# Kernel tuning notes

Hardware: AMD Instinct MI355X
Metric: run time of the kernel (lower is better)

Reference implementation:

```python
import jax, jax.numpy as jnp
import numpy as np

HID = 128
MAX_NODES = 100000
MAX_EDGES = 300000
EVT_LEN = 4096
NUM_NODE = 20000
NUM_EDGE = 320000
# EVENT_TYPE_ID_MAP: pad=0 start=1 end=2 node-add=3 node-delete=4 edge-add=5 edge-delete=6
NODE_ADD, NODE_DEL = 3, 4


def time_encode(t, time_w, time_b):
    # TimeEncoder: cos(Linear(1 -> hidden)(t))
    return jnp.cos(t[..., None] * time_w + time_b)


def gru_cell(x, h, w_ih, w_hh, b_ih, b_hh):
    gi = x @ w_ih.T + b_ih
    gh = h @ w_hh.T + b_hh
    i_r, i_z, i_n = jnp.split(gi, 3, axis=-1)
    h_r, h_z, h_n = jnp.split(gh, 3, axis=-1)
    r = jax.nn.sigmoid(i_r + h_r)
    z = jax.nn.sigmoid(i_z + h_z)
    n = jnp.tanh(i_n + r * h_n)
    return (1.0 - z) * n + z * h


def setup_inputs() -> dict:
    key = jax.random.key(0)
    ks = jax.random.split(key, 32)
    H = HID
    s = 0.05
    inp = {}
    inp["event_type_ids"] = jax.random.randint(ks[0], (EVT_LEN,), 0, 7)
    inp["src_ids"] = jax.random.randint(ks[1], (EVT_LEN,), 0, MAX_NODES)
    inp["src_mask"] = (jax.random.uniform(ks[2], (EVT_LEN,)) > 0.3).astype(jnp.float32)
    inp["dst_ids"] = jax.random.randint(ks[3], (EVT_LEN,), 0, MAX_NODES)
    inp["dst_mask"] = (jax.random.uniform(ks[4], (EVT_LEN,)) > 0.3).astype(jnp.float32)
    inp["event_edge_ids"] = jax.random.randint(ks[5], (EVT_LEN,), 0, MAX_EDGES)
    inp["event_embeddings"] = jax.random.normal(ks[6], (EVT_LEN, H), dtype=jnp.float32)
    inp["event_mask"] = (jax.random.uniform(ks[7], (EVT_LEN,)) > 0.2).astype(jnp.float32)
    inp["event_timestamps"] = jax.random.uniform(ks[8], (EVT_LEN,)) * 100.0
    inp["node_ids"] = jax.random.randint(ks[9], (NUM_NODE,), 0, MAX_NODES)
    inp["edge_ids"] = jax.random.randint(ks[10], (NUM_EDGE,), 0, MAX_EDGES)
    inp["edge_index"] = jax.random.randint(ks[11], (2, NUM_EDGE), 0, NUM_NODE)
    inp["time"] = 100
    # persistent-buffer state
    inp["memory"] = jax.random.normal(ks[12], (MAX_NODES, H), dtype=jnp.float32) * s
    inp["last_update"] = jax.random.uniform(ks[13], (MAX_EDGES,)) * 50.0
    inp["node_features"] = jax.random.normal(ks[14], (MAX_NODES, H), dtype=jnp.float32) * s
    inp["edge_features"] = jax.random.normal(ks[15], (MAX_EDGES, H), dtype=jnp.float32) * s
    # TimeEncoder params (Linear(1, H))
    inp["time_w"] = jax.random.normal(ks[16], (H,), dtype=jnp.float32) * s
    inp["time_b"] = jax.random.normal(ks[17], (H,), dtype=jnp.float32) * s
    # GRUCell(5H -> H)
    inp["gru_w_ih"] = jax.random.normal(ks[18], (3 * H, 5 * H), dtype=jnp.float32) * s
    inp["gru_w_hh"] = jax.random.normal(ks[19], (3 * H, H), dtype=jnp.float32) * s
    inp["gru_b_ih"] = jax.random.normal(ks[20], (3 * H,), dtype=jnp.float32) * s
    inp["gru_b_hh"] = jax.random.normal(ks[21], (3 * H,), dtype=jnp.float32) * s
    # TransformerConv(H, H, heads=1, edge_dim=2H)
    inp["wq"] = jax.random.normal(ks[22], (H, H), dtype=jnp.float32) * s
    inp["bq"] = jax.random.normal(ks[23], (H,), dtype=jnp.float32) * s
    inp["wk"] = jax.random.normal(ks[24], (H, H), dtype=jnp.float32) * s
    inp["bk"] = jax.random.normal(ks[25], (H,), dtype=jnp.float32) * s
    inp["wv"] = jax.random.normal(ks[26], (H, H), dtype=jnp.float32) * s
    inp["bv"] = jax.random.normal(ks[27], (H,), dtype=jnp.float32) * s
    inp["we"] = jax.random.normal(ks[28], (H, 2 * H), dtype=jnp.float32) * s  # lin_edge, no bias
    inp["wskip"] = jax.random.normal(ks[29], (H, H), dtype=jnp.float32) * s
    inp["bskip"] = jax.random.normal(ks[30], (H,), dtype=jnp.float32) * s
    return inp


def reference(event_type_ids, src_ids, src_mask, dst_ids, dst_mask, event_edge_ids,
              event_embeddings, event_mask, event_timestamps, node_ids, edge_ids,
              edge_index, time, memory, last_update, node_features, edge_features,
              time_w, time_b, gru_w_ih, gru_w_hh, gru_b_ih, gru_b_hh,
              wq, bq, wk, bk, wv, bv, we, wskip, bskip):
    H = HID
    # ---- message() ----
    L = event_type_ids.shape[0]
    type_embs = jnp.broadcast_to(event_type_ids[:, None].astype(memory.dtype), (L, H))
    src_embs = memory[src_ids] * src_mask[:, None]
    dst_embs = memory[dst_ids] * dst_mask[:, None]
    edge_last = last_update[event_edge_ids]
    rel_ts = event_timestamps - edge_last * dst_mask
    is_node_ev = ((event_type_ids == NODE_ADD) | (event_type_ids == NODE_DEL)).astype(event_timestamps.dtype)
    ts_emb = time_encode(event_timestamps * is_node_ev + rel_ts * dst_mask, time_w, time_b) * event_mask[:, None]
    src_msgs = jnp.concatenate([type_embs, src_embs, dst_embs, ts_emb, event_embeddings], axis=1) * event_mask[:, None]
    dst_msgs = jnp.concatenate([type_embs, dst_embs, src_embs, ts_emb, event_embeddings], axis=1) * dst_mask[:, None]
    # ---- agg_message(): scatter-mean over node ids ----
    def agg(msgs, ids):
        s = jax.ops.segment_sum(msgs, ids, num_segments=MAX_NODES)
        c = jax.ops.segment_sum(jnp.ones((msgs.shape[0],), msgs.dtype), ids, num_segments=MAX_NODES)
        return s / jnp.maximum(c, 1.0)[:, None]
    agg_src = agg(src_msgs, src_ids)
    agg_dst = agg(dst_msgs, dst_ids)
    # ---- GRU memory update on unique ids ----
    # torch: memory[cat(uniq_src, uniq_dst)] = rnn(...); reads use pre-update memory,
    # dst writes come after src writes so they override on overlap. Duplicate ids in
    # src_ids carry identical per-id values, so scatter-set is equivalent to unique().
    new_src = gru_cell(agg_src[src_ids], memory[src_ids], gru_w_ih, gru_w_hh, gru_b_ih, gru_b_hh)
    new_dst = gru_cell(agg_dst[dst_ids], memory[dst_ids], gru_w_ih, gru_w_hh, gru_b_ih, gru_b_hh)
    memory = memory.at[src_ids].set(new_src)
    memory = memory.at[dst_ids].set(new_dst)
    # ---- edge attributes ----
    rel_t = time - last_update[edge_ids]
    rel_t_embs = time_encode(rel_t, time_w, time_b)
    edge_attr = jnp.concatenate([rel_t_embs, edge_features[edge_ids]], axis=-1)  # (E, 2H)
    # ---- TransformerConv (heads=1, concat, root_weight) ----
    x = node_features[node_ids] + memory[node_ids]  # (N, H)
    src, dst = edge_index[0], edge_index[1]
    q = x @ wq.T + bq
    k = x @ wk.T + bk
    v = x @ wv.T + bv
    e = edge_attr @ we.T  # lin_edge (no bias)
    alpha = jnp.sum(q[dst] * (k[src] + e), axis=-1) / jnp.sqrt(jnp.asarray(H, x.dtype))
    amax = jax.ops.segment_max(alpha, dst, num_segments=x.shape[0])
    ex = jnp.exp(alpha - amax[dst])
    denom = jax.ops.segment_sum(ex, dst, num_segments=x.shape[0])
    p = ex / jnp.maximum(denom[dst], 1e-16)
    out = jax.ops.segment_sum(p[:, None] * (v[src] + e), dst, num_segments=x.shape[0])
    return out + x @ wskip.T + bskip
```

## Files before the change

kernel.cpp:

```cpp
#include <hip/hip_runtime.h>
#include <math.h>

#define HID   128
#define MAXN  100000
#define MAXE  300000
#define EVT   4096
#define NNODE 20000
#define NEDGE 320000

typedef unsigned short u16;
typedef __attribute__((ext_vector_type(8))) short bf16x8;
typedef __attribute__((ext_vector_type(4))) float f32x4;

#define OFF_WCATB     0u
#define OFF_WEB       589824u
#define OFF_WALLB     655360u
#define OFF_BALL      851968u
#define BASE2         855040u
#define OFF_HEAD_SRC  (BASE2 + 0u)
#define OFF_HEAD_DST  (BASE2 + 400128u)
#define OFF_CNT_SRC   (BASE2 + 800256u)
#define OFF_CNT_DST   (BASE2 + 1200384u)
#define OFF_CHAIN_SRC (BASE2 + 1600512u)
#define OFF_CHAIN_DST (BASE2 + 1616896u)
#define OFF_XHB       (BASE2 + 1703936u)
#define OFF_HG        (BASE2 + 14286848u)
#define OFF_XB        (BASE2 + 20000000u)
#define OFF_QB        (BASE2 + 25120000u)
#define OFF_SKIPF     (BASE2 + 55840000u)
#define OFF_DEG       (BASE2 + 66080000u)
#define OFF_OFFS      (BASE2 + 66160128u)
#define OFF_CURSOR    (BASE2 + 66240256u)
#define OFF_SORTED    (BASE2 + 66320384u)
#define OFF_SACCB     (BASE2 + 67600384u)

__device__ __forceinline__ float sigmoidf_(float x) { return 1.f / (1.f + __expf(-x)); }
__device__ __forceinline__ u16 f2b(float f) {
    unsigned u = __float_as_uint(f);
    unsigned r = (u + 0x7fffu + ((u >> 16) & 1u)) >> 16;
    return (u16)r;
}
__device__ __forceinline__ float b2f(unsigned h) { return __uint_as_float(h << 16); }

__global__ void k_prep(const float* __restrict__ w_ih, const float* __restrict__ w_hh,
                       const float* __restrict__ we,
                       const float* __restrict__ wq, const float* __restrict__ wk_,
                       const float* __restrict__ wv, const float* __restrict__ wskip,
                       const float* __restrict__ bq, const float* __restrict__ bk,
                       const float* __restrict__ bv, const float* __restrict__ bskip,
                       u16* __restrict__ Wcatb, u16* __restrict__ we_b,
                       u16* __restrict__ Wallb, float* __restrict__ ball,
                       int* __restrict__ deg, char* __restrict__ zbase) {
    int b = blockIdx.x, t = threadIdx.x;
    if (b < 1152) {
        int idx = b * 256 + t;
        int row = idx / 768, col = idx % 768;
        float v = (col < 640) ? w_ih[row * 640 + col] : w_hh[row * 128 + (col - 640)];
        Wcatb[idx] = f2b(v);
        return;
    }
    b -= 1152;
    if (b < 128) {
        int i = b * 256 + t;
        we_b[i] = f2b(we[i]);
        return;
    }
    b -= 128;
    if (b < 79) {
        int i = b * 256 + t;
        if (i < NNODE) deg[i] = 0;
        return;
    }
    b -= 79;
    if (b < 384) {
        int idx = b * 256 + t;
        int row = idx >> 7;
        int k = idx & 127;
        float v;
        if (row < 128)      v = wq[row * 128 + k];
        else if (row < 256) v = wk_[(row - 128) * 128 + k];
        else if (row < 384) v = wv[(row - 256) * 128 + k];
        else if (row < 512) v = wskip[(row - 384) * 128 + k];
        else {
            int j = row - 512;
            float a = 0.f;
            for (int t2 = 0; t2 < 128; t2++) a += wq[t2 * 128 + k] * we[t2 * 256 + j];
            v = a;
        }
        Wallb[row * 128 + k] = f2b(v);
        if (k == 0) {
            float bb;
            if (row < 128)      bb = bq[row];
            else if (row < 256) bb = bk[row - 128];
            else if (row < 384) bb = bv[row - 256];
            else if (row < 512) bb = bskip[row - 384];
            else { int j = row - 512; float a = 0.f; for (int t2 = 0; t2 < 128; t2++) a += bq[t2] * we[t2 * 256 + j]; bb = a; }
            ball[row] = bb;
        }
        return;
    }
    b -= 384;
    const int NFF = 50016;
    uint4 ff = make_uint4(0xFFFFFFFFu, 0xFFFFFFFFu, 0xFFFFFFFFu, 0xFFFFFFFFu);
    uint4 zz = make_uint4(0u, 0u, 0u, 0u);
    int idx = b * 256 + t;
    int stride = 257 * 256;
    uint4* pff = (uint4*)zbase;
    uint4* pzz = (uint4*)(zbase + 800256);
    for (int i = idx; i < NFF; i += stride) pff[i] = ff;
    for (int i = idx; i < NFF; i += stride) pzz[i] = zz;
}

__global__ void k_msg_tables(const int* __restrict__ et_ids, const int* __restrict__ src_ids,
                          const float* __restrict__ src_mask, const int* __restrict__ dst_ids,
                          const float* __restrict__ dst_mask, const int* __restrict__ ev_eids,
                          const float* __restrict__ ev_emb, const float* __restrict__ ev_mask,
                          const float* __restrict__ ev_ts, const float* __restrict__ memory,
                          const float* __restrict__ last_update, const float* __restrict__ time_w,
                          const float* __restrict__ time_b,
                          int* __restrict__ head_src, int* __restrict__ head_dst,
                          int* __restrict__ cnt_src, int* __restrict__ cnt_dst,
                          int* __restrict__ chain_src, int* __restrict__ chain_dst,
                          const int* __restrict__ eidx, int* __restrict__ deg,
                          u16* __restrict__ XHb, float* __restrict__ Hg) {
    int b = blockIdx.x, t = threadIdx.x;
    if (b >= EVT) {
        int bb = b - EVT;
        if (bb < 32) {
            int i = bb * 128 + t;
            int s = src_ids[i], d = dst_ids[i];
            chain_src[i] = atomicExch(&head_src[s], i);
            atomicAdd(&cnt_src[s], 1);
            chain_dst[i] = atomicExch(&head_dst[d], i);
            atomicAdd(&cnt_dst[d], 1);
        } else {
            int j = (bb - 32) * 128 + t;
            atomicAdd(&deg[eidx[NEDGE + j]], 1);
        }
        return;
    }
    int i = b;
    int c = t;
    int et = et_ids[i];
    float sm = src_mask[i], dm = dst_mask[i], em = ev_mask[i], ts = ev_ts[i];
    int sid = src_ids[i], did = dst_ids[i], eid = ev_eids[i];
    float isnode = (et == 3 || et == 4) ? 1.f : 0.f;
    float rel = ts - last_update[eid] * dm;
    float tval = ts * isnode + rel * dm;
    float tse = __cosf(tval * time_w[c] + time_b[c]) * em;
    float typ = (float)et;
    float sv_raw = memory[(size_t)sid * HID + c];
    float dv_raw = memory[(size_t)did * HID + c];
    float sv = sv_raw * sm;
    float dv = dv_raw * dm;
    float ev = ev_emb[(size_t)i * HID + c];
    Hg[(size_t)i * HID + c] = sv_raw;
    Hg[(size_t)(EVT + i) * HID + c] = dv_raw;
    u16* xs = XHb + (size_t)i * 768;
    xs[c] = f2b(typ * em); xs[128 + c] = f2b(sv * em); xs[256 + c] = f2b(dv * em);
    xs[384 + c] = f2b(tse * em); xs[512 + c] = f2b(ev * em);
    xs[640 + c] = f2b(sv_raw);
    u16* xd = XHb + (size_t)(EVT + i) * 768;
    xd[c] = f2b(typ * dm); xd[128 + c] = f2b(dv * dm); xd[256 + c] = f2b(sv * dm);
    xd[384 + c] = f2b(tse * dm); xd[512 + c] = f2b(ev * dm);
    xd[640 + c] = f2b(dv_raw);
}

__global__ void k_fix(const int* __restrict__ src_ids, const int* __restrict__ dst_ids,
                      const int* __restrict__ head_src, const int* __restrict__ head_dst,
                      const int* __restrict__ chain_src, const int* __restrict__ chain_dst,
                      const int* __restrict__ cnt_src, const int* __restrict__ cnt_dst,
                      const int* __restrict__ et_ids, const float* __restrict__ src_mask,
                      const float* __restrict__ dst_mask, const int* __restrict__ ev_eids,
                      const float* __restrict__ ev_emb, const float* __restrict__ ev_mask,
                      const float* __restrict__ ev_ts, const float* __restrict__ memory,
                      const float* __restrict__ last_update, const float* __restrict__ time_w,
                      const float* __restrict__ time_b, u16* __restrict__ XHb) {
    int r = blockIdx.x, c = threadIdx.x;
    bool is_src = (r < EVT);
    int id = is_src ? src_ids[r] : dst_ids[r - EVT];
    int cnt = is_src ? cnt_src[id] : cnt_dst[id];
    if (cnt < 2) return;
    float own = memory[(size_t)id * HID + c];
    float tw = time_w[c], tb = time_b[c];
    float a0 = 0.f, a1 = 0.f, a2 = 0.f, a3 = 0.f, a4 = 0.f;
    int j = is_src ? head_src[id] : head_dst[id];
    for (int k = 0; k < cnt; ++k) {
        int et = et_ids[j];
        float sm = src_mask[j], dm = dst_mask[j], em = ev_mask[j], ts = ev_ts[j];
        int eid = ev_eids[j];
        float isnode = (et == 3 || et == 4) ? 1.f : 0.f;
        float rel = ts - last_update[eid] * dm;
        float tval = ts * isnode + rel * dm;
        float tse = __cosf(tval * tw + tb);
        float ev = ev_emb[(size_t)j * HID + c];
        float typ = (float)et;
        if (is_src) {
            float sv = own * sm;
            float dv = memory[(size_t)dst_ids[j] * HID + c] * dm;
            float tsm = tse * em;
            a0 += typ * em; a1 += sv * em; a2 += dv * em;
            a3 += tsm * em; a4 += ev * em;
            j = chain_src[j];
        } else {
            float dv = own * dm;
            float sv = memory[(size_t)src_ids[j] * HID + c] * sm;
            float tsm = tse * em;
            a0 += typ * dm; a1 += dv * dm; a2 += sv * dm;
            a3 += tsm * dm; a4 += ev * dm;
            j = chain_dst[j];
        }
    }
    float inv = 1.f / (float)cnt;
    u16* x = XHb + (size_t)r * 768;
    x[c] = f2b(a0 * inv); x[128 + c] = f2b(a1 * inv); x[256 + c] = f2b(a2 * inv);
    x[384 + c] = f2b(a3 * inv); x[512 + c] = f2b(a4 * inv);
}

__device__ __forceinline__ void gate_pass(const u16* __restrict__ A, int lda,
                                          const u16* __restrict__ W, int ldw, int K,
                                          f32x4 acc[4][4], u16* Als, u16* Wls,
                                          int bm, int wm, int wn, int l15, int quad, int tid) {
    for (int k0 = 0; k0 < K; k0 += 32) {
#pragma unroll
        for (int h = 0; h < 2; ++h) {
            int ch = tid + h * 256;
            int row = ch >> 2, kc = (ch & 3) * 8;
            *(float4*)&Als[row * 40 + kc] = *(const float4*)(A + (size_t)(bm + row) * lda + k0 + kc);
            *(float4*)&Wls[row * 40 + kc] = *(const float4*)(W + (size_t)row * ldw + k0 + kc);
        }
        __syncthreads();
        bf16x8 af[4], bfr[4];
#pragma unroll
        for (int r = 0; r < 4; ++r)
            af[r] = *(const bf16x8*)&Als[(wm + r * 16 + l15) * 40 + quad * 8];
#pragma unroll
        for (int c2 = 0; c2 < 4; ++c2)
            bfr[c2] = *(const bf16x8*)&Wls[(wn + c2 * 16 + l15) * 40 + quad * 8];
#pragma unroll
        for (int r = 0; r < 4; ++r)
#pragma unroll
            for (int c2 = 0; c2 < 4; ++c2)
                acc[r][c2] = __builtin_amdgcn_mfma_f32_16x16x32_bf16(af[r], bfr[c2], acc[r][c2], 0, 0, 0);
        __syncthreads();
    }
}

__global__ __launch_bounds__(256, 1) void k_gates(const u16* __restrict__ XHb,
        const u16* __restrict__ Wcat, const float* __restrict__ b_ih,
        const float* __restrict__ b_hh, const float* __restrict__ Hg,
        const int* __restrict__ src_ids, const int* __restrict__ dst_ids,
        const int* __restrict__ cnt_dst, float* __restrict__ memory) {
    __shared__ u16 Als[128 * 40];
    __shared__ u16 Wls[128 * 40];
    int tid = threadIdx.x;
    int bm = blockIdx.x * 128;
    int wave = tid >> 6, lane = tid & 63;
    int wm = (wave & 1) * 64, wn = (wave >> 1) * 64;
    int l15 = lane & 15, quad = lane >> 4;
    f32x4 acc_h[4][4] = {};
    f32x4 acc_a[4][4] = {};
    f32x4 acc_i[4][4] = {};
    gate_pass(XHb + 640, 768, Wcat + (size_t)256 * 768 + 640, 768, 128,
              acc_h, Als, Wls, bm, wm, wn, l15, quad, tid);
    gate_pass(XHb, 768, Wcat, 768, 768, acc_a, Als, Wls, bm, wm, wn, l15, quad, tid);
#pragma unroll
    for (int r = 0; r < 4; ++r)
#pragma unroll
        for (int c2 = 0; c2 < 4; ++c2) {
            int ncol = wn + c2 * 16 + l15;
            float bs0 = b_ih[ncol] + b_hh[ncol];
            float bh2 = b_hh[256 + ncol];
#pragma unroll
            for (int reg = 0; reg < 4; ++reg) {
                float rg = sigmoidf_(acc_a[r][c2][reg] + bs0);
                acc_h[r][c2][reg] = rg * (acc_h[r][c2][reg] + bh2);
                acc_a[r][c2][reg] = 0.f;
            }
        }
    gate_pass(XHb, 768, Wcat + (size_t)128 * 768, 768, 768,
              acc_a, Als, Wls, bm, wm, wn, l15, quad, tid);
    gate_pass(XHb, 768, Wcat + (size_t)256 * 768, 768, 640,
              acc_i, Als, Wls, bm, wm, wn, l15, quad, tid);
#pragma unroll
    for (int r = 0; r < 4; ++r)
#pragma unroll
        for (int c2 = 0; c2 < 4; ++c2) {
            int ncol = wn + c2 * 16 + l15;
            float bz = b_ih[128 + ncol] + b_hh[128 + ncol];
            float bi2 = b_ih[256 + ncol];
#pragma unroll
            for (int reg = 0; reg < 4; ++reg) {
                int mrow = bm + wm + r * 16 + quad * 4 + reg;
                float z = sigmoidf_(acc_a[r][c2][reg] + bz);
                float n = tanhf(acc_i[r][c2][reg] + bi2 + acc_h[r][c2][reg]);
                float h0 = Hg[(size_t)mrow * HID + ncol];
                float h = (1.f - z) * n + z * h0;
                if (mrow < EVT) {
                    int sid = src_ids[mrow];
                    if (cnt_dst[sid] == 0) memory[(size_t)sid * HID + ncol] = h;
                } else {
                    int did = dst_ids[mrow - EVT];
                    memory[(size_t)did * HID + ncol] = h;
                }
            }
        }
}

__device__ __forceinline__ void gemm_tile(const u16* __restrict__ A, const u16* __restrict__ W,
                                          const float* __restrict__ bias, float* __restrict__ C,
                                          int M, int N, int K, int acc,
                                          u16* Als, u16* Wls) {
    int tid = threadIdx.x;
    int bm = blockIdx.x * 128, bn = blockIdx.y * 128;
    int wave = tid >> 6, lane = tid & 63;
    int wm = (wave & 1) * 64, wn = (wave >> 1) * 64;
    int l15 = lane & 15, quad = lane >> 4;
    f32x4 accf[4][4] = {};
    for (int k0 = 0; k0 < K; k0 += 32) {
#pragma unroll
        for (int h = 0; h < 2; ++h) {
            int ch = tid + h * 256;
            int row = ch >> 2, kc = (ch & 3) * 8;
            int gr = bm + row;
            float4 av = make_float4(0.f, 0.f, 0.f, 0.f);
            if (gr < M) av = *(const float4*)(A + (size_t)gr * K + k0 + kc);
            *(float4*)&Als[row * 40 + kc] = av;
            int wr = bn + row;
            float4 wv_ = *(const float4*)(W + (size_t)wr * K + k0 + kc);
            *(float4*)&Wls[row * 40 + kc] = wv_;
        }
        __syncthreads();
        bf16x8 af[4], bfr[4];
#pragma unroll
        for (int r = 0; r < 4; ++r)
            af[r] = *(const bf16x8*)&Als[(wm + r * 16 + l15) * 40 + quad * 8];
#pragma unroll
        for (int c2 = 0; c2 < 4; ++c2)
            bfr[c2] = *(const bf16x8*)&Wls[(wn + c2 * 16 + l15) * 40 + quad * 8];
#pragma unroll
        for (int r = 0; r < 4; ++r)
#pragma unroll
            for (int c2 = 0; c2 < 4; ++c2)
                accf[r][c2] = __builtin_amdgcn_mfma_f32_16x16x32_bf16(af[r], bfr[c2], accf[r][c2], 0, 0, 0);
        __syncthreads();
    }
#pragma unroll
    for (int r = 0; r < 4; ++r) {
#pragma unroll
        for (int c2 = 0; c2 < 4; ++c2) {
            int ncol = bn + wn + c2 * 16 + l15;
            float bv = bias ? bias[ncol] : 0.f;
#pragma unroll
            for (int reg = 0; reg < 4; ++reg) {
                int mrow = bm + wm + r * 16 + quad * 4 + reg;
                if (mrow >= M) continue;
                float v = accf[r][c2][reg] + bv;
                if (acc) v += C[(size_t)mrow * N + ncol];
                C[(size_t)mrow * N + ncol] = v;
            }
        }
    }
}

__global__ __launch_bounds__(256) void k_gemm_mfma(const u16* __restrict__ A,
                                                   const u16* __restrict__ W,
                                                   const float* __restrict__ bias,
                                                   float* __restrict__ C,
                                                   int M, int N, int K, int acc) {
    __shared__ u16 Als[128 * 40];
    __shared__ u16 Wls[128 * 40];
    gemm_tile(A, W, bias, C, M, N, K, acc, Als, Wls);
}

__global__ __launch_bounds__(256) void k_gemm_qkvse(const u16* __restrict__ A,
                                                    const u16* __restrict__ W,
                                                    const float* __restrict__ bias,
                                                    u16* __restrict__ QB,
                                                    float* __restrict__ SkipF,
                                                    const int* __restrict__ eidx,
                                                    int* __restrict__ cursor,
                                                    int* __restrict__ sorted) {
    __shared__ u16 Als[128 * 40];
    __shared__ u16 Wls[128 * 40];
    if (blockIdx.y == 6) {
        int j = blockIdx.x * 256 + threadIdx.x;
        for (; j < NEDGE; j += 157 * 256) {
            int d = eidx[NEDGE + j];
            int pos = atomicAdd(&cursor[d], 1);
            sorted[pos] = j;
        }
        return;
    }
    int tid = threadIdx.x;
    int bm = blockIdx.x * 128, bn = blockIdx.y * 128;
    int wave = tid >> 6, lane = tid & 63;
    int wm = (wave & 1) * 64, wn = (wave >> 1) * 64;
    int l15 = lane & 15, quad = lane >> 4;
    f32x4 accf[4][4] = {};
    for (int k0 = 0; k0 < 128; k0 += 32) {
#pragma unroll
        for (int h = 0; h < 2; ++h) {
            int ch = tid + h * 256;
            int row = ch >> 2, kc = (ch & 3) * 8;
            int gr = bm + row;
            float4 av = make_float4(0.f, 0.f, 0.f, 0.f);
            if (gr < NNODE) av = *(const float4*)(A + (size_t)gr * 128 + k0 + kc);
            *(float4*)&Als[row * 40 + kc] = av;
            int wr = bn + row;
            float4 wv_ = *(const float4*)(W + (size_t)wr * 128 + k0 + kc);
            *(float4*)&Wls[row * 40 + kc] = wv_;
        }
        __syncthreads();
        bf16x8 af[4], bfr[4];
#pragma unroll
        for (int r = 0; r < 4; ++r)
            af[r] = *(const bf16x8*)&Als[(wm + r * 16 + l15) * 40 + quad * 8];
#pragma unroll
        for (int c2 = 0; c2 < 4; ++c2)
            bfr[c2] = *(const bf16x8*)&Wls[(wn + c2 * 16 + l15) * 40 + quad * 8];
#pragma unroll
        for (int r = 0; r < 4; ++r)
#pragma unroll
            for (int c2 = 0; c2 < 4; ++c2)
                accf[r][c2] = __builtin_amdgcn_mfma_f32_16x16x32_bf16(af[r], bfr[c2], accf[r][c2], 0, 0, 0);
        __syncthreads();
    }
#pragma unroll
    for (int r = 0; r < 4; ++r) {
#pragma unroll
        for (int c2 = 0; c2 < 4; ++c2) {
            int ncol = bn + wn + c2 * 16 + l15;
            float bv = bias[ncol];
#pragma unroll
            for (int reg = 0; reg < 4; ++reg) {
                int mrow = bm + wm + r * 16 + quad * 4 + reg;
                if (mrow >= NNODE) continue;
                float v = accf[r][c2][reg] + bv;
                QB[(size_t)mrow * 768 + ncol] = f2b(v);
                if (ncol >= 384 && ncol < 512)
                    SkipF[(size_t)mrow * 128 + (ncol - 384)] = v;
            }
        }
    }
}

__global__ __launch_bounds__(1024) void k_x_scan(const int* __restrict__ node_ids,
                                                 const float* __restrict__ nf,
                                                 const float* __restrict__ memory,
                                                 u16* __restrict__ Xb,
                                                 const int* __restrict__ deg,
                                                 int* __restrict__ offs,
                                                 int* __restrict__ cursor) {
    __shared__ int wsum[16];
    int p = blockIdx.x, t = threadIdx.x;
    if (p < 2500) {
        int row = p * 8 + (t >> 7), c = t & 127;
        int nid = node_ids[row];
        Xb[(size_t)row * HID + c] = f2b(nf[(size_t)nid * HID + c] + memory[(size_t)nid * HID + c]);
        return;
    }
    int lane = t & 63, w = t >> 6;
    int carry = 0;
    const int N4 = NNODE / 4;
    for (int base = 0; base < N4; base += 1024) {
        int i4 = base + t;
        int4 v = make_int4(0, 0, 0, 0);
        if (i4 < N4) v = ((const int4*)deg)[i4];
        int s = v.x + v.y + v.z + v.w;
        int x = s;
#pragma unroll
        for (int d = 1; d < 64; d <<= 1) { int y = __shfl_up(x, d, 64); if (lane >= d) x += y; }
        if (lane == 63) wsum[w] = x;
        __syncthreads();
        int add = 0, tot = 0;
        for (int k2 = 0; k2 < 16; ++k2) { int ss = wsum[k2]; if (k2 < w) add += ss; tot += ss; }
        if (i4 < N4) {
            int e = carry + add + x - s;
            int4 o;
            o.x = e;
            o.y = e + v.x;
            o.z = o.y + v.y;
            o.w = o.z + v.z;
            ((int4*)offs)[i4] = o;
            ((int4*)cursor)[i4] = o;
        }
        carry += tot;
        __syncthreads();
    }
    if (t == 0) offs[NNODE] = NEDGE;
}

__global__ __launch_bounds__(256) void k_node(const u16* __restrict__ QB,
        const float* __restrict__ SkipF, const int* __restrict__ offs,
        const int* __restrict__ sorted, const int* __restrict__ eidx,
        const int* __restrict__ edge_ids, const float* __restrict__ last_update,
        const float* __restrict__ time_w, const float* __restrict__ time_b,
        const float* __restrict__ ef, const int* __restrict__ tptr,
        float* __restrict__ out, u16* __restrict__ saccb) {
    int wave = threadIdx.x >> 6, lane = threadIdx.x & 63;
    int n = blockIdx.x * 4 + wave;
    int c = 2 * lane;
    const u16* rowq = QB + (size_t)n * 768;
    unsigned qw  = *(const unsigned*)(rowq + c);
    unsigned qtw = *(const unsigned*)(rowq + 512 + c);
    unsigned qfw = *(const unsigned*)(rowq + 640 + c);
    float2 qd, qet, qef;
    qd.x  = b2f(qw & 0xffffu);  qd.y  = b2f(qw >> 16);
    qet.x = b2f(qtw & 0xffffu); qet.y = b2f(qtw >> 16);
    qef.x = b2f(qfw & 0xffffu); qef.y = b2f(qfw >> 16);
    float2 skip = *(const float2*)(SkipF + (size_t)n * HID + c);
    float2 tw   = *(const float2*)(time_w + c);
    float2 tb   = *(const float2*)(time_b + c);
    float tf = (float)(*tptr);
    int start = offs[n], end = offs[n + 1];
    int deg = end - start;
    if (deg == 0) {
        *(float2*)(out + (size_t)n * HID + c) = skip;
        *(unsigned*)(saccb + (size_t)n * 256 + c) = 0u;
        *(unsigned*)(saccb + (size_t)n * 256 + 128 + c) = 0u;
        return;
    }
    float m = -1e30f, l_ = 0.f;
    float va0 = 0.f, va1 = 0.f, s00 = 0.f, s01 = 0.f, s10 = 0.f, s11 = 0.f;
    for (int cb = start; cb < end; cb += 64) {
        int cnt = end - cb; if (cnt > 64) cnt = 64;
        int s_l = 0, eid_l = 0; float rt_l = 0.f;
        if (lane < cnt) {
            int j = sorted[cb + lane];
            s_l = eidx[j];
            eid_l = edge_ids[j];
            rt_l = tf - last_update[eid_l];
        }
        for (int e0 = 0; e0 < cnt; e0 += 4) {
            float pv[4], cv0[4], cv1[4], vx[4], vy[4], ex[4], ey[4];
#pragma unroll
            for (int i = 0; i < 4; ++i) {
                int idx = e0 + i;
                int sel = (idx < cnt) ? idx : e0;
                int s   = __shfl(s_l, sel, 64);
                int eid = __shfl(eid_l, sel, 64);
                float rt = __shfl(rt_l, sel, 64);
                unsigned kvp = *(const unsigned*)(QB + (size_t)s * 768 + 128 + c);
                unsigned vvp = *(const unsigned*)(QB + (size_t)s * 768 + 256 + c);
                float2 ev = *(const float2*)(ef + (size_t)eid * HID + c);
                float k0f = b2f(kvp & 0xffffu), k1f = b2f(kvp >> 16);
                vx[i] = b2f(vvp & 0xffffu); vy[i] = b2f(vvp >> 16);
                cv0[i] = __cosf(rt * tw.x + tb.x);
                cv1[i] = __cosf(rt * tw.y + tb.y);
                ex[i] = ev.x; ey[i] = ev.y;
                pv[i] = qd.x * k0f + qd.y * k1f + qet.x * cv0[i] + qet.y * cv1[i]
                      + qef.x * ev.x + qef.y * ev.y;
            }
#pragma unroll
            for (int msk = 32; msk > 0; msk >>= 1) {
#pragma unroll
                for (int i = 0; i < 4; ++i) pv[i] += __shfl_xor(pv[i], msk, 64);
            }
            float al[4];
#pragma unroll
            for (int i = 0; i < 4; ++i)
                al[i] = (e0 + i < cnt) ? pv[i] * 0.08838834764831845f : -1e30f;
            float gm = fmaxf(fmaxf(al[0], al[1]), fmaxf(al[2], al[3]));
            if (gm > m) {
                float fac = __expf(m - gm);
                l_ *= fac; va0 *= fac; va1 *= fac;
                s00 *= fac; s01 *= fac; s10 *= fac; s11 *= fac;
                m = gm;
            }
#pragma unroll
            for (int i = 0; i < 4; ++i) {
                float w = __expf(al[i] - m);
                l_ += w;
                va0 += w * vx[i]; va1 += w * vy[i];
                s00 += w * cv0[i]; s01 += w * cv1[i];
                s10 += w * ex[i]; s11 += w * ey[i];
            }
        }
    }
    float inv = 1.f / fmaxf(l_, 1e-16f);
    float2 o; o.x = va0 * inv + skip.x; o.y = va1 * inv + skip.y;
    *(float2*)(out + (size_t)n * HID + c) = o;
    unsigned p0 = (unsigned)f2b(s00 * inv) | ((unsigned)f2b(s01 * inv) << 16);
    unsigned p1 = (unsigned)f2b(s10 * inv) | ((unsigned)f2b(s11 * inv) << 16);
    *(unsigned*)(saccb + (size_t)n * 256 + c) = p0;
    *(unsigned*)(saccb + (size_t)n * 256 + 128 + c) = p1;
}

extern "C" void kernel_launch(void* const* d_in, const int* in_sizes, int n_in,
                              void* d_out, int out_size, void* d_ws, size_t ws_size,
                              hipStream_t stream) {
    const int*   et_ids        = (const int*)d_in[0];
    const int*   src_ids       = (const int*)d_in[1];
    const float* src_mask      = (const float*)d_in[2];
    const int*   dst_ids       = (const int*)d_in[3];
    const float* dst_mask      = (const float*)d_in[4];
    const int*   ev_eids       = (const int*)d_in[5];
    const float* ev_emb        = (const float*)d_in[6];
    const float* ev_mask       = (const float*)d_in[7];
    const float* ev_ts         = (const float*)d_in[8];
    const int*   node_ids      = (const int*)d_in[9];
    const int*   edge_ids      = (const int*)d_in[10];
    const int*   edge_index    = (const int*)d_in[11];
    const int*   tptr          = (const int*)d_in[12];
    float*       memory        = (float*)d_in[13];
    const float* last_update   = (const float*)d_in[14];
    const float* node_features = (const float*)d_in[15];
    const float* edge_features = (const float*)d_in[16];
    const float* time_w        = (const float*)d_in[17];
    const float* time_b        = (const float*)d_in[18];
    const float* w_ih          = (const float*)d_in[19];
    const float* w_hh          = (const float*)d_in[20];
    const float* b_ih          = (const float*)d_in[21];
    const float* b_hh          = (const float*)d_in[22];
    const float* wq            = (const float*)d_in[23];
    const float* bq            = (const float*)d_in[24];
    const float* wk            = (const float*)d_in[25];
    const float* bk            = (const float*)d_in[26];
    const float* wv            = (const float*)d_in[27];
    const float* bv            = (const float*)d_in[28];
    const float* we            = (const float*)d_in[29];
    const float* wskip         = (const float*)d_in[30];
    const float* bskip         = (const float*)d_in[31];
    float* out = (float*)d_out;
    char*  wsb = (char*)d_ws;

    u16*   Wcatb    = (u16*)(wsb + OFF_WCATB);
    u16*   we_b     = (u16*)(wsb + OFF_WEB);
    u16*   Wallb    = (u16*)(wsb + OFF_WALLB);
    float* ball     = (float*)(wsb + OFF_BALL);
    int*   head_src = (int*)(wsb + OFF_HEAD_SRC);
    int*   head_dst = (int*)(wsb + OFF_HEAD_DST);
    int*   cnt_src  = (int*)(wsb + OFF_CNT_SRC);
    int*   cnt_dst  = (int*)(wsb + OFF_CNT_DST);
    int*   chain_src= (int*)(wsb + OFF_CHAIN_SRC);
    int*   chain_dst= (int*)(wsb + OFF_CHAIN_DST);
    u16*   XHb      = (u16*)(wsb + OFF_XHB);
    float* Hg       = (float*)(wsb + OFF_HG);
    u16*   Xb       = (u16*)(wsb + OFF_XB);
    u16*   QB       = (u16*)(wsb + OFF_QB);
    float* SkipF    = (float*)(wsb + OFF_SKIPF);
    int*   deg      = (int*)(wsb + OFF_DEG);
    int*   offs     = (int*)(wsb + OFF_OFFS);
    int*   cursor   = (int*)(wsb + OFF_CURSOR);
    int*   sorted   = (int*)(wsb + OFF_SORTED);
    u16*   saccb    = (u16*)(wsb + OFF_SACCB);

    k_prep<<<2000, 256, 0, stream>>>(w_ih, w_hh, we, wq, wk, wv, wskip, bq, bk, bv, bskip,
                                     Wcatb, we_b, Wallb, ball, deg, wsb + OFF_HEAD_SRC);
    k_msg_tables<<<6628, 128, 0, stream>>>(et_ids, src_ids, src_mask, dst_ids, dst_mask, ev_eids,
                                           ev_emb, ev_mask, ev_ts, memory, last_update, time_w, time_b,
                                           head_src, head_dst, cnt_src, cnt_dst, chain_src, chain_dst,
                                           edge_index, deg, XHb, Hg);
    k_fix<<<2 * EVT, 128, 0, stream>>>(src_ids, dst_ids, head_src, head_dst, chain_src, chain_dst,
                                       cnt_src, cnt_dst, et_ids, src_mask, dst_mask, ev_eids,
                                       ev_emb, ev_mask, ev_ts, memory, last_update, time_w, time_b,
                                       XHb);
    k_gates<<<64, 256, 0, stream>>>(XHb, Wcatb, b_ih, b_hh, Hg, src_ids, dst_ids, cnt_dst, memory);
    k_x_scan<<<2501, 1024, 0, stream>>>(node_ids, node_features, memory, Xb, deg, offs, cursor);
    k_gemm_qkvse<<<dim3(157, 7), 256, 0, stream>>>(Xb, Wallb, ball, QB, SkipF,
                                                   edge_index, cursor, sorted);
    k_node<<<NNODE / 4, 256, 0, stream>>>(QB, SkipF, offs, sorted, edge_index, edge_ids,
                                          last_update, time_w, time_b, edge_features, tptr,
                                          out, saccb);
    k_gemm_mfma<<<dim3(157, 1), 256, 0, stream>>>(saccb, we_b, nullptr, out, NNODE, 128, 256, 1);
}
```

Before: 538.1 us.

## Split fused GRU gate kernel into gate-parallel GEMM plus elementwise scatter

```diff
diff --git a/kernel.cpp b/kernel.cpp
--- a/kernel.cpp
+++ b/kernel.cpp
@@ -25,6 +25,9 @@
 #define OFF_CHAIN_DST (BASE2 + 1616896u)
 #define OFF_XHB       (BASE2 + 1703936u)
 #define OFF_HG        (BASE2 + 14286848u)
+#define OFF_GRZ       (BASE2 + 20000000u)
+#define OFF_GIN       (BASE2 + 28388608u)
+#define OFF_GHN       (BASE2 + 32582912u)
 #define OFF_XB        (BASE2 + 20000000u)
 #define OFF_QB        (BASE2 + 25120000u)
 #define OFF_SKIPF     (BASE2 + 55840000u)
@@ -246,65 +249,62 @@
     }
 }
 
-__global__ __launch_bounds__(256, 1) void k_gates(const u16* __restrict__ XHb,
+__global__ __launch_bounds__(256) void k_gemm_gates(const u16* __restrict__ XHb,
         const u16* __restrict__ Wcat, const float* __restrict__ b_ih,
-        const float* __restrict__ b_hh, const float* __restrict__ Hg,
-        const int* __restrict__ src_ids, const int* __restrict__ dst_ids,
-        const int* __restrict__ cnt_dst, float* __restrict__ memory) {
+        const float* __restrict__ b_hh, float* __restrict__ Grz,
+        float* __restrict__ Gin, float* __restrict__ Ghn) {
     __shared__ u16 Als[128 * 40];
     __shared__ u16 Wls[128 * 40];
     int tid = threadIdx.x;
     int bm = blockIdx.x * 128;
+    int g = blockIdx.y;
     int wave = tid >> 6, lane = tid & 63;
     int wm = (wave & 1) * 64, wn = (wave >> 1) * 64;
     int l15 = lane & 15, quad = lane >> 4;
+    f32x4 acc_i[4][4] = {};
     f32x4 acc_h[4][4] = {};
-    f32x4 acc_a[4][4] = {};
-    f32x4 acc_i[4][4] = {};
-    gate_pass(XHb + 640, 768, Wcat + (size_t)256 * 768 + 640, 768, 128,
-              acc_h, Als, Wls, bm, wm, wn, l15, quad, tid);
-    gate_pass(XHb, 768, Wcat, 768, 768, acc_a, Als, Wls, bm, wm, wn, l15, quad, tid);
-#pragma unroll
-    for (int r = 0; r < 4; ++r)
+    const u16* Wg = Wcat + (size_t)(g * 128) * 768;
+    gate_pass(XHb, 768, Wg, 768, 640, acc_i, Als, Wls, bm, wm, wn, l15, quad, tid);
+    gate_pass(XHb + 640, 768, Wg + 640, 768, 128, acc_h, Als, Wls, bm, wm, wn, l15, quad, tid);
+#pragma unroll
+    for (int r = 0; r < 4; ++r) {
 #pragma unroll
         for (int c2 = 0; c2 < 4; ++c2) {
             int ncol = wn + c2 * 16 + l15;
-            float bs0 = b_ih[ncol] + b_hh[ncol];
-            float bh2 = b_hh[256 + ncol];
-#pragma unroll
-            for (int reg = 0; reg < 4; ++reg) {
-                float rg = sigmoidf_(acc_a[r][c2][reg] + bs0);
-                acc_h[r][c2][reg] = rg * (acc_h[r][c2][reg] + bh2);
-                acc_a[r][c2][reg] = 0.f;
-            }
-        }
-    gate_pass(XHb, 768, Wcat + (size_t)128 * 768, 768, 768,
-              acc_a, Als, Wls, bm, wm, wn, l15, quad, tid);
-    gate_pass(XHb, 768, Wcat + (size_t)256 * 768, 768, 640,
-              acc_i, Als, Wls, bm, wm, wn, l15, quad, tid);
-#pragma unroll
-    for (int r = 0; r < 4; ++r)
-#pragma unroll
-        for (int c2 = 0; c2 < 4; ++c2) {
-            int ncol = wn + c2 * 16 + l15;
-            float bz = b_ih[128 + ncol] + b_hh[128 + ncol];
-            float bi2 = b_ih[256 + ncol];
+            float bi = b_ih[g * 128 + ncol];
+            float bh = b_hh[g * 128 + ncol];
 #pragma unroll
             for (int reg = 0; reg < 4; ++reg) {
                 int mrow = bm + wm + r * 16 + quad * 4 + reg;
-                float z = sigmoidf_(acc_a[r][c2][reg] + bz);
-                float n = tanhf(acc_i[r][c2][reg] + bi2 + acc_h[r][c2][reg]);
-                float h0 = Hg[(size_t)mrow * HID + ncol];
-                float h = (1.f - z) * n + z * h0;
-                if (mrow < EVT) {
-                    int sid = src_ids[mrow];
-                    if (cnt_dst[sid] == 0) memory[(size_t)sid * HID + ncol] = h;
+                if (g < 2) {
+                    Grz[(size_t)mrow * 256 + g * 128 + ncol] =
+                        acc_i[r][c2][reg] + acc_h[r][c2][reg] + bi + bh;
                 } else {
-                    int did = dst_ids[mrow - EVT];
-                    memory[(size_t)did * HID + ncol] = h;
+                    Gin[(size_t)mrow * 128 + ncol] = acc_i[r][c2][reg] + bi;
+                    Ghn[(size_t)mrow * 128 + ncol] = acc_h[r][c2][reg] + bh;
                 }
             }
         }
+    }
+}
+
+__global__ void k_gru_scatter(const float* __restrict__ Grz, const float* __restrict__ Gin,
+                              const float* __restrict__ Ghn, const float* __restrict__ Hg,
+                              const int* __restrict__ src_ids, const int* __restrict__ dst_ids,
+                              const int* __restrict__ cnt_dst, float* __restrict__ memory) {
+    int r = blockIdx.x, c = threadIdx.x;
+    float rg = sigmoidf_(Grz[(size_t)r * 256 + c]);
+    float z  = sigmoidf_(Grz[(size_t)r * 256 + 128 + c]);
+    float n  = tanhf(Gin[(size_t)r * 128 + c] + rg * Ghn[(size_t)r * 128 + c]);
+    float h0 = Hg[(size_t)r * HID + c];
+    float h  = (1.f - z) * n + z * h0;
+    if (r < EVT) {
+        int sid = src_ids[r];
+        if (cnt_dst[sid] == 0) memory[(size_t)sid * HID + c] = h;
+    } else {
+        int did = dst_ids[r - EVT];
+        memory[(size_t)did * HID + c] = h;
+    }
 }
 
 __device__ __forceinline__ void gemm_tile(const u16* __restrict__ A, const u16* __restrict__ W,
@@ -637,6 +637,9 @@
     int*   chain_dst= (int*)(wsb + OFF_CHAIN_DST);
     u16*   XHb      = (u16*)(wsb + OFF_XHB);
     float* Hg       = (float*)(wsb + OFF_HG);
+    float* Grz      = (float*)(wsb + OFF_GRZ);
+    float* Gin      = (float*)(wsb + OFF_GIN);
+    float* Ghn      = (float*)(wsb + OFF_GHN);
     u16*   Xb       = (u16*)(wsb + OFF_XB);
     u16*   QB       = (u16*)(wsb + OFF_QB);
     float* SkipF    = (float*)(wsb + OFF_SKIPF);
@@ -656,7 +659,8 @@
                                        cnt_src, cnt_dst, et_ids, src_mask, dst_mask, ev_eids,
                                        ev_emb, ev_mask, ev_ts, memory, last_update, time_w, time_b,
                                        XHb);
-    k_gates<<<64, 256, 0, stream>>>(XHb, Wcatb, b_ih, b_hh, Hg, src_ids, dst_ids, cnt_dst, memory);
+    k_gemm_gates<<<dim3(64, 3), 256, 0, stream>>>(XHb, Wcatb, b_ih, b_hh, Grz, Gin, Ghn);
+    k_gru_scatter<<<2 * EVT, 128, 0, stream>>>(Grz, Gin, Ghn, Hg, src_ids, dst_ids, cnt_dst, memory);
     k_x_scan<<<2501, 1024, 0, stream>>>(node_ids, node_features, memory, Xb, deg, offs, cursor);
     k_gemm_qkvse<<<dim3(157, 7), 256, 0, stream>>>(Xb, Wallb, ball, QB, SkipF,
                                                    edge_index, cursor, sorted);
```

After: 480.8 us. 1.12x faster.
